# Kernel optimization log

Measured on AMD Instinct MI355X. Metric: run time of the kernel, lower is better.

Reference implementation:

```python
import jax, jax.numpy as jnp
import numpy as np

B, T, D_IN, D_H = 64, 4096, 128, 128


def setup_inputs() -> dict:
    key = jax.random.key(0)
    k1, k2, k3 = jax.random.split(key, 3)
    x = jax.random.normal(k1, (B, T, D_IN), dtype=jnp.float32)
    # Glorot-ish scaling so tanh does not saturate over 4096 steps
    W_x = jax.random.normal(k2, (D_IN, D_H), dtype=jnp.float32) / jnp.sqrt(D_IN)
    W_h = jax.random.normal(k3, (D_H, D_H), dtype=jnp.float32) / jnp.sqrt(D_H)
    b = jnp.zeros((D_H,), dtype=jnp.float32)
    return {"x": x, "W_x": W_x, "W_h": W_h, "b": b}


def reference(x, W_x, W_h, b):
    """CellWrapper: scan a vanilla tanh RNN cell over the time axis of x.

    x: (B, T, D_in)  ->  outputs: (B, T, D_h)
    h_t = tanh(x_t @ W_x + h_{t-1} @ W_h + b), h_0 = 0 (as in init_h).
    """
    init_h = jnp.zeros((x.shape[0], W_h.shape[0]), dtype=x.dtype)  # (B, D_h)

    def step(h, x_t):
        h_new = jnp.tanh(x_t @ W_x + h @ W_h + b)
        return h_new, h_new

    # scan is time-major; swap to (T, B, D_in) and back
    _, ys = jax.lax.scan(step, init_h, jnp.swapaxes(x, 0, 1))
    return jnp.swapaxes(ys, 0, 1)  # (B, T, D_h)
```

## Files before the change

### kernel.cpp

```cpp
#include <hip/hip_runtime.h>
#include <cmath>

#define BB   64
#define TT   4096
#define DIN  128
#define DH   128
#define GROWS 64

typedef float v2f __attribute__((ext_vector_type(2)));
typedef float v4f __attribute__((ext_vector_type(4)));

__device__ __forceinline__ void pk_fma(v2f& acc, v2f a, v2f b) {
    asm("v_pk_fma_f32 %0, %1, %2, %0" : "+v"(acc) : "v"(a), "v"(b));
}

__device__ __forceinline__ float fast_tanh(float x) {
    float e = exp2f(x * 2.885390081777927f);
    float r = __builtin_amdgcn_rcpf(e + 1.0f);
    return __builtin_fmaf(-2.0f, r, 1.0f);
}

__global__ __launch_bounds__(256, 2) void xwx_gemm(const float* __restrict__ x,
                                                   const float* __restrict__ Wx,
                                                   const float* __restrict__ bias,
                                                   float* __restrict__ P) {
    __shared__ v4f xs4[GROWS * DIN / 4];
    const int tid = threadIdx.x;
    const size_t row0 = (size_t)blockIdx.x * GROWS;

    const v4f* xg = (const v4f*)x + row0 * (DIN / 4);
#pragma unroll
    for (int i = 0; i < (GROWS * DIN / 4) / 256; ++i)
        xs4[tid + i * 256] = xg[tid + i * 256];

    const int j  = tid & (DH - 1);
    const int rg = tid >> 7;

    v2f wj2[DIN / 2];
#pragma unroll
    for (int m = 0; m < DIN / 2; ++m) {
        v2f w;
        w.x = Wx[(2 * m + 0) * DH + j];
        w.y = Wx[(2 * m + 1) * DH + j];
        wj2[m] = w;
        asm("" : "+v"(wj2[m]));
    }
    const float bj = bias[j];

    __syncthreads();

#pragma unroll 1
    for (int r = 0; r < GROWS / 2; ++r) {
        const v4f* xr = xs4 + (rg * (GROWS / 2) + r) * (DIN / 4);
        v2f a0 = {0.f, 0.f}, a1 = {0.f, 0.f}, a2 = {0.f, 0.f}, a3 = {0.f, 0.f};
#pragma unroll
        for (int k4 = 0; k4 < DIN / 4; k4 += 2) {
            v4f ha = xr[k4];
            v4f hb = xr[k4 + 1];
            v2f ha01 = {ha.x, ha.y}, ha23 = {ha.z, ha.w};
            v2f hb01 = {hb.x, hb.y}, hb23 = {hb.z, hb.w};
            pk_fma(a0, ha01, wj2[2 * k4 + 0]);
            pk_fma(a1, ha23, wj2[2 * k4 + 1]);
            pk_fma(a2, hb01, wj2[2 * k4 + 2]);
            pk_fma(a3, hb23, wj2[2 * k4 + 3]);
        }
        float s = ((a0.x + a0.y) + (a1.x + a1.y)) + ((a2.x + a2.y) + (a3.x + a3.y));
        P[(row0 + rg * (GROWS / 2) + r) * DH + j] = s + bj;
    }
}

__global__ __launch_bounds__(128, 1) void rnn_scan(float* po,
                                                   const float* __restrict__ Wh) {
    const int b = blockIdx.x;
    const int j = threadIdx.x;

    __shared__ v4f hbuf[2][DH / 4];

    v2f wj2[DH / 2];
#pragma unroll
    for (int m = 0; m < DH / 2; ++m) {
        v2f w;
        w.x = Wh[(2 * m + 0) * DH + j];
        w.y = Wh[(2 * m + 1) * DH + j];
        wj2[m] = w;
        asm("" : "+v"(wj2[m]));
    }

    float* pbB = po + (size_t)b * TT * DH + j;

    float pc[8], pn[8];
#pragma unroll
    for (int i = 0; i < 8; ++i) pc[i] = pbB[(size_t)i * DH];

    ((float*)hbuf[0])[j] = 0.f;
    __syncthreads();

    int cur = 0;
#pragma unroll 1
    for (int tg = 0; tg < TT; tg += 8) {
#pragma unroll
        for (int i = 0; i < 8; ++i) {
            int tl = tg + 8 + i;
            tl = (tl < TT) ? tl : (TT - 1);
            pn[i] = pbB[(size_t)tl * DH];
        }

#pragma unroll
        for (int u = 0; u < 8; ++u) {
            const int t = tg + u;
            const v4f* h4 = hbuf[cur];
            v2f a0 = {pc[u], 0.f}, a1 = {0.f, 0.f}, a2 = {0.f, 0.f}, a3 = {0.f, 0.f};
#pragma unroll
            for (int k4 = 0; k4 < DH / 4; k4 += 2) {
                v4f ha = h4[k4];
                v4f hb = h4[k4 + 1];
                v2f ha01 = {ha.x, ha.y}, ha23 = {ha.z, ha.w};
                v2f hb01 = {hb.x, hb.y}, hb23 = {hb.z, hb.w};
                pk_fma(a0, ha01, wj2[2 * k4 + 0]);
                pk_fma(a1, ha23, wj2[2 * k4 + 1]);
                pk_fma(a2, hb01, wj2[2 * k4 + 2]);
                pk_fma(a3, hb23, wj2[2 * k4 + 3]);
            }
            float s = ((a0.x + a0.y) + (a1.x + a1.y)) + ((a2.x + a2.y) + (a3.x + a3.y));
            float hnew = fast_tanh(s);

            pbB[(size_t)t * DH] = hnew;
            ((float*)hbuf[cur ^ 1])[j] = hnew;

            asm volatile("s_waitcnt lgkmcnt(0)\n\ts_barrier" ::: "memory");
            cur ^= 1;
        }

#pragma unroll
        for (int i = 0; i < 8; ++i) pc[i] = pn[i];
    }
}

extern "C" void kernel_launch(void* const* d_in, const int* in_sizes, int n_in,
                              void* d_out, int out_size, void* d_ws, size_t ws_size,
                              hipStream_t stream) {
    const float* x    = (const float*)d_in[0];
    const float* Wx   = (const float*)d_in[1];
    const float* Wh   = (const float*)d_in[2];
    const float* bias = (const float*)d_in[3];
    float* out = (float*)d_out;

    const int nblk = (BB * TT) / GROWS;
    xwx_gemm<<<nblk, 256, 0, stream>>>(x, Wx, bias, out);

    rnn_scan<<<BB, 128, 0, stream>>>(out, Wh);
}
```

Before: 2.294 ms.

## Run RNN scan in a single wavefront without barriers, double-buffer GEMM chunks

The recurrent scan now runs on one 64-lane wavefront per batch row, with each lane computing two hidden units using packed FMAs with op_sel broadcast. Because only one wave touches the shared h buffer, the per-step s_barrier is dropped and only an LDS waitcnt remains, which removes workgroup synchronisation from the serial critical path. The cost is twice the FMA work per lane and 256 weight registers per lane. Separately, the input GEMM processes four row chunks per block and prefetches the next chunk into a second LDS buffer, so the weight-loading setup is amortised over more rows.

```diff
diff --git a/kernel.cpp b/kernel.cpp
--- a/kernel.cpp
+++ b/kernel.cpp
@@ -5,13 +5,22 @@
 #define TT   4096
 #define DIN  128
 #define DH   128
-#define GROWS 64
+#define GROWS  64
+#define NCHUNK 4
 
 typedef float v2f __attribute__((ext_vector_type(2)));
 typedef float v4f __attribute__((ext_vector_type(4)));
 
 __device__ __forceinline__ void pk_fma(v2f& acc, v2f a, v2f b) {
     asm("v_pk_fma_f32 %0, %1, %2, %0" : "+v"(acc) : "v"(a), "v"(b));
+}
+__device__ __forceinline__ void pk_fma_blo(v2f& acc, v2f a, v2f b) {
+    asm("v_pk_fma_f32 %0, %1, %2, %0 op_sel:[0,0,0] op_sel_hi:[0,1,1]"
+        : "+v"(acc) : "v"(a), "v"(b));
+}
+__device__ __forceinline__ void pk_fma_bhi(v2f& acc, v2f a, v2f b) {
+    asm("v_pk_fma_f32 %0, %1, %2, %0 op_sel:[1,0,0] op_sel_hi:[1,1,1]"
+        : "+v"(acc) : "v"(a), "v"(b));
 }
 
 __device__ __forceinline__ float fast_tanh(float x) {
@@ -24,14 +33,9 @@
                                                    const float* __restrict__ Wx,
                                                    const float* __restrict__ bias,
                                                    float* __restrict__ P) {
-    __shared__ v4f xs4[GROWS * DIN / 4];
+    __shared__ v4f xs4[2][GROWS * DIN / 4];
     const int tid = threadIdx.x;
-    const size_t row0 = (size_t)blockIdx.x * GROWS;
-
-    const v4f* xg = (const v4f*)x + row0 * (DIN / 4);
-#pragma unroll
-    for (int i = 0; i < (GROWS * DIN / 4) / 256; ++i)
-        xs4[tid + i * 256] = xg[tid + i * 256];
+    const size_t row0 = (size_t)blockIdx.x * (GROWS * NCHUNK);
 
     const int j  = tid & (DH - 1);
     const int rg = tid >> 7;
@@ -39,81 +43,39 @@
     v2f wj2[DIN / 2];
 #pragma unroll
     for (int m = 0; m < DIN / 2; ++m) {
-        v2f w;
-        w.x = Wx[(2 * m + 0) * DH + j];
-        w.y = Wx[(2 * m + 1) * DH + j];
-        wj2[m] = w;
-        asm("" : "+v"(wj2[m]));
+        wj2[m].x = Wx[(2 * m + 0) * DH + j];
+        wj2[m].y = Wx[(2 * m + 1) * DH + j];
     }
+#pragma unroll
+    for (int m = 0; m < DIN / 2; ++m) asm("" : "+v"(wj2[m]));
     const float bj = bias[j];
 
+    {
+        const v4f* xg = (const v4f*)x + row0 * (DIN / 4);
+#pragma unroll
+        for (int i = 0; i < (GROWS * DIN / 4) / 256; ++i)
+            xs4[0][tid + i * 256] = xg[tid + i * 256];
+    }
     __syncthreads();
 
 #pragma unroll 1
-    for (int r = 0; r < GROWS / 2; ++r) {
-        const v4f* xr = xs4 + (rg * (GROWS / 2) + r) * (DIN / 4);
-        v2f a0 = {0.f, 0.f}, a1 = {0.f, 0.f}, a2 = {0.f, 0.f}, a3 = {0.f, 0.f};
+    for (int c = 0; c < NCHUNK; ++c) {
+        if (c + 1 < NCHUNK) {
+            const v4f* xg = (const v4f*)x + (row0 + (size_t)(c + 1) * GROWS) * (DIN / 4);
 #pragma unroll
-        for (int k4 = 0; k4 < DIN / 4; k4 += 2) {
-            v4f ha = xr[k4];
-            v4f hb = xr[k4 + 1];
-            v2f ha01 = {ha.x, ha.y}, ha23 = {ha.z, ha.w};
-            v2f hb01 = {hb.x, hb.y}, hb23 = {hb.z, hb.w};
-            pk_fma(a0, ha01, wj2[2 * k4 + 0]);
-            pk_fma(a1, ha23, wj2[2 * k4 + 1]);
-            pk_fma(a2, hb01, wj2[2 * k4 + 2]);
-            pk_fma(a3, hb23, wj2[2 * k4 + 3]);
-        }
-        float s = ((a0.x + a0.y) + (a1.x + a1.y)) + ((a2.x + a2.y) + (a3.x + a3.y));
-        P[(row0 + rg * (GROWS / 2) + r) * DH + j] = s + bj;
-    }
-}
-
-__global__ __launch_bounds__(128, 1) void rnn_scan(float* po,
-                                                   const float* __restrict__ Wh) {
-    const int b = blockIdx.x;
-    const int j = threadIdx.x;
-
-    __shared__ v4f hbuf[2][DH / 4];
-
-    v2f wj2[DH / 2];
-#pragma unroll
-    for (int m = 0; m < DH / 2; ++m) {
-        v2f w;
-        w.x = Wh[(2 * m + 0) * DH + j];
-        w.y = Wh[(2 * m + 1) * DH + j];
-        wj2[m] = w;
-        asm("" : "+v"(wj2[m]));
-    }
-
-    float* pbB = po + (size_t)b * TT * DH + j;
-
-    float pc[8], pn[8];
-#pragma unroll
-    for (int i = 0; i < 8; ++i) pc[i] = pbB[(size_t)i * DH];
-
-    ((float*)hbuf[0])[j] = 0.f;
-    __syncthreads();
-
-    int cur = 0;
-#pragma unroll 1
-    for (int tg = 0; tg < TT; tg += 8) {
-#pragma unroll
-        for (int i = 0; i < 8; ++i) {
-            int tl = tg + 8 + i;
-            tl = (tl < TT) ? tl : (TT - 1);
-            pn[i] = pbB[(size_t)tl * DH];
+            for (int i = 0; i < (GROWS * DIN / 4) / 256; ++i)
+                xs4[(c + 1) & 1][tid + i * 256] = xg[tid + i * 256];
         }
 
+        const size_t r0 = row0 + (size_t)c * GROWS;
+#pragma unroll 1
+        for (int r = 0; r < GROWS / 2; ++r) {
+            const v4f* xr = xs4[c & 1] + (rg * (GROWS / 2) + r) * (DIN / 4);
+            v2f a0 = {0.f, 0.f}, a1 = {0.f, 0.f}, a2 = {0.f, 0.f}, a3 = {0.f, 0.f};
 #pragma unroll
-        for (int u = 0; u < 8; ++u) {
-            const int t = tg + u;
-            const v4f* h4 = hbuf[cur];
-            v2f a0 = {pc[u], 0.f}, a1 = {0.f, 0.f}, a2 = {0.f, 0.f}, a3 = {0.f, 0.f};
-#pragma unroll
-            for (int k4 = 0; k4 < DH / 4; k4 += 2) {
-                v4f ha = h4[k4];
-                v4f hb = h4[k4 + 1];
+            for (int k4 = 0; k4 < DIN / 4; k4 += 2) {
+                v4f ha = xr[k4];
+                v4f hb = xr[k4 + 1];
                 v2f ha01 = {ha.x, ha.y}, ha23 = {ha.z, ha.w};
                 v2f hb01 = {hb.x, hb.y}, hb23 = {hb.z, hb.w};
                 pk_fma(a0, ha01, wj2[2 * k4 + 0]);
@@ -122,13 +84,64 @@
                 pk_fma(a3, hb23, wj2[2 * k4 + 3]);
             }
             float s = ((a0.x + a0.y) + (a1.x + a1.y)) + ((a2.x + a2.y) + (a3.x + a3.y));
-            float hnew = fast_tanh(s);
+            P[(r0 + rg * (GROWS / 2) + r) * DH + j] = s + bj;
+        }
+        __syncthreads();
+    }
+}
 
-            pbB[(size_t)t * DH] = hnew;
-            ((float*)hbuf[cur ^ 1])[j] = hnew;
+__global__ __launch_bounds__(64, 1) void rnn_scan(float* po,
+                                                  const float* __restrict__ Wh) {
+    const int b = blockIdx.x;
+    const int l = threadIdx.x;
 
-            asm volatile("s_waitcnt lgkmcnt(0)\n\ts_barrier" ::: "memory");
-            cur ^= 1;
+    __shared__ alignas(16) v2f hbuf[2][DH / 2];
+
+    v2f w[DH];
+#pragma unroll
+    for (int k = 0; k < DH; ++k)
+        w[k] = *(const v2f*)(Wh + (size_t)k * DH + 2 * l);
+#pragma unroll
+    for (int k = 0; k < DH; ++k) asm("" : "+v"(w[k]));
+
+    float* pbase = po + (size_t)b * TT * DH + 2 * l;
+
+    v2f pc[8], pn[8];
+#pragma unroll
+    for (int i = 0; i < 8; ++i) pc[i] = *(const v2f*)(pbase + (size_t)i * DH);
+
+    hbuf[0][l] = v2f{0.f, 0.f};
+    asm volatile("s_waitcnt lgkmcnt(0)" ::: "memory");
+
+#pragma unroll 1
+    for (int tg = 0; tg < TT; tg += 8) {
+#pragma unroll
+        for (int i = 0; i < 8; ++i) {
+            int tl = tg + 8 + i;
+            tl = (tl < TT) ? tl : (TT - 1);
+            pn[i] = *(const v2f*)(pbase + (size_t)tl * DH);
+        }
+
+#pragma unroll
+        for (int u = 0; u < 8; ++u) {
+            const v4f* h4 = (const v4f*)hbuf[u & 1];
+            v2f a0 = {pc[u].x, pc[u].y}, a1 = {0.f, 0.f}, a2 = {0.f, 0.f}, a3 = {0.f, 0.f};
+#pragma unroll
+            for (int q = 0; q < DH / 4; ++q) {
+                v4f hv = h4[q];
+                v2f h01 = {hv.x, hv.y};
+                v2f h23 = {hv.z, hv.w};
+                pk_fma_blo(a0, h01, w[4 * q + 0]);
+                pk_fma_bhi(a1, h01, w[4 * q + 1]);
+                pk_fma_blo(a2, h23, w[4 * q + 2]);
+                pk_fma_bhi(a3, h23, w[4 * q + 3]);
+            }
+            v2f s2 = (a0 + a1) + (a2 + a3);
+            v2f hnew = {fast_tanh(s2.x), fast_tanh(s2.y)};
+
+            *(v2f*)(pbase + (size_t)(tg + u) * DH) = hnew;
+            hbuf[(u + 1) & 1][l] = hnew;
+            asm volatile("s_waitcnt lgkmcnt(0)" ::: "memory");
         }
 
 #pragma unroll
@@ -145,8 +158,8 @@
     const float* bias = (const float*)d_in[3];
     float* out = (float*)d_out;
 
-    const int nblk = (BB * TT) / GROWS;
+    const int nblk = (BB * TT) / (GROWS * NCHUNK);
     xwx_gemm<<<nblk, 256, 0, stream>>>(x, Wx, bias, out);
 
-    rnn_scan<<<BB, 128, 0, stream>>>(out, Wh);
+    rnn_scan<<<BB, 64, 0, stream>>>(out, Wh);
 }
```

After: 7.265 ms. 3.17x slower.
